# Kernel optimization log

Measured on AMD Instinct MI355X. Metric: run time of the kernel, lower is better.

Reference implementation:

```python
import jax, jax.numpy as jnp
import numpy as np

B, C, H, W = 4, 32, 64, 64
D_STATE, D_CONV = 16, 4


def _mamba(x, Win, convw, convb, Wx, Wdt, dtb, Alog, D, Wout, dt_rank):
    Bsz, L, _ = x.shape
    d_in, K = convw.shape
    xz = x @ Win.T                                  # (B, L, 2*d_inner)
    xc, z = xz[..., :d_in], xz[..., d_in:]
    xp = jnp.pad(xc, ((0, 0), (K - 1, 0), (0, 0)))  # causal left pad
    xconv = convb + sum(convw[:, k] * xp[:, k:k + L, :] for k in range(K))
    xa = jax.nn.silu(xconv)                         # (B, L, d_inner)
    xdbl = xa @ Wx.T                                # (B, L, dt_rank + 2*N)
    dt = jax.nn.softplus(xdbl[..., :dt_rank] @ Wdt.T + dtb)     # (B, L, d_inner)
    Bm = xdbl[..., dt_rank:dt_rank + D_STATE]                   # (B, L, N)
    Cm = xdbl[..., dt_rank + D_STATE:]                          # (B, L, N)
    A = -jnp.exp(Alog)                                          # (d_inner, N)
    dA = jnp.exp(dt[..., None] * A)                             # (B, L, d_inner, N)
    dBu = dt[..., None] * Bm[:, :, None, :] * xa[..., None]     # (B, L, d_inner, N)

    def step(h, inp):
        dA_t, dBu_t, C_t = inp
        h = dA_t * h + dBu_t
        return h, jnp.einsum('bdn,bn->bd', h, C_t)

    h0 = jnp.zeros((Bsz, d_in, D_STATE), x.dtype)
    _, ys = jax.lax.scan(step, h0, (dA.transpose(1, 0, 2, 3), dBu.transpose(1, 0, 2, 3), Cm.transpose(1, 0, 2)))
    y = ys.transpose(1, 0, 2) + D * xa
    return (y * jax.nn.silu(z)) @ Wout.T


def _line_seqs(x):
    # x: (B,C,H,W) -> four (B, H*W, C) directional scan orders
    hf = x.reshape(B, C, H * W).transpose(0, 2, 1)
    hb = hf[:, ::-1, :]
    wf = x.transpose(0, 1, 3, 2).reshape(B, C, H * W).transpose(0, 2, 1)
    wb = wf[:, ::-1, :]
    return hf, hb, wf, wb


def _oss(fo1, fo2, p1, p2):
    hf, hb, wf, wb = _line_seqs(fo1)
    fop = jnp.concatenate([hf, hb, wf, wb], axis=2)       # (B, HW, 4C)
    fop = _mamba(fop, *p1, dt_rank=8)
    fop = fop.reshape(B, H * W, 4, C).sum(2)              # (B, HW, C)
    fop = fop.transpose(0, 2, 1).reshape(B, C, H, W)
    residual = fop * fo2
    foc = residual.mean(axis=(2, 3)).reshape(B, C, 1)     # adaptive_avg_pool2d (1,1)
    foc = jnp.concatenate([foc, foc[:, ::-1, :]], axis=2) # (B, C, 2)
    foc = _mamba(foc, *p2, dt_rank=1)
    foc = foc.sum(2, keepdims=True)[..., None]            # (B, C, 1, 1)
    return foc * residual + residual


def setup_inputs() -> dict:
    key = jax.random.key(0)
    ks = jax.random.split(key, 18)
    def n(k, shape, s=0.02):
        return jax.random.normal(k, shape, jnp.float32) * s
    dm1, di1, dr1 = 4 * C, 8 * C, 8
    dm2, di2, dr2 = 2, 4, 1
    return {
        'fo1': jax.random.normal(ks[0], (B, C, H, W), jnp.float32),
        'fo2': jax.random.normal(ks[1], (B, C, H, W), jnp.float32),
        'm1_Win': n(ks[2], (2 * di1, dm1)),
        'm1_convw': n(ks[3], (di1, D_CONV), 0.2),
        'm1_convb': n(ks[4], (di1,), 0.1),
        'm1_Wx': n(ks[5], (dr1 + 2 * D_STATE, di1)),
        'm1_Wdt': n(ks[6], (di1, dr1), 0.1),
        'm1_dtb': n(ks[7], (di1,), 0.5),
        'm1_Alog': jnp.log(jnp.tile(jnp.arange(1, D_STATE + 1, dtype=jnp.float32), (di1, 1))),
        'm1_D': jnp.ones((di1,), jnp.float32),
        'm1_Wout': n(ks[8], (dm1, di1)),
        'm2_Win': n(ks[9], (2 * di2, dm2)),
        'm2_convw': n(ks[10], (di2, D_CONV), 0.2),
        'm2_convb': n(ks[11], (di2,), 0.1),
        'm2_Wx': n(ks[12], (dr2 + 2 * D_STATE, di2)),
        'm2_Wdt': n(ks[13], (di2, dr2), 0.1),
        'm2_dtb': n(ks[14], (di2,), 0.5),
        'm2_Alog': jnp.log(jnp.tile(jnp.arange(1, D_STATE + 1, dtype=jnp.float32), (di2, 1))),
        'm2_D': jnp.ones((di2,), jnp.float32),
        'm2_Wout': n(ks[15], (dm2, di2)),
    }


def reference(fo1, fo2, m1_Win, m1_convw, m1_convb, m1_Wx, m1_Wdt, m1_dtb, m1_Alog, m1_D, m1_Wout,
              m2_Win, m2_convw, m2_convb, m2_Wx, m2_Wdt, m2_dtb, m2_Alog, m2_D, m2_Wout):
    p1 = (m1_Win, m1_convw, m1_convb, m1_Wx, m1_Wdt, m1_dtb, m1_Alog, m1_D, m1_Wout)
    p2 = (m2_Win, m2_convw, m2_convb, m2_Wx, m2_Wdt, m2_dtb, m2_Alog, m2_D, m2_Wout)
    return _oss(fo1, fo2, p1, p2)
```

## Files before the change

kernel.cpp:

```cpp
#include <hip/hip_runtime.h>
#include <cstddef>


typedef __attribute__((ext_vector_type(8))) short short8v;
typedef __attribute__((ext_vector_type(4))) float f32x4;

__device__ __forceinline__ float siluf(float x) { return x / (1.f + __expf(-x)); }
__device__ __forceinline__ float softplusf(float x) { return (x > 20.f) ? x : log1pf(__expf(x)); }
__device__ __forceinline__ unsigned short f2bf(float f) {
  union { float f; unsigned int u; } v; v.f = f;
  unsigned int r = v.u + 0x7fff + ((v.u >> 16) & 1);
  return (unsigned short)(r >> 16);
}
__device__ __forceinline__ float bf2f(unsigned short u) {
  union { unsigned int i; float f; } v; v.i = ((unsigned int)u) << 16; return v.f;
}

__global__ __launch_bounds__(256) void k_build_fop(const float* __restrict__ fo1,
                                                   unsigned short* __restrict__ fopb) {
  int idx = blockIdx.x * 256 + threadIdx.x;
  int j = idx & 127;
  int l = (idx >> 7) & 4095;
  int b = idx >> 19;
  int g = j >> 5, c = j & 31;
  const float* base = fo1 + (size_t)(b * 32 + c) * 4096;
  int li;
  if (g == 0)      li = l;
  else if (g == 1) li = 4095 - l;
  else if (g == 2) li = ((l & 63) << 6) + (l >> 6);
  else { int i2 = 4095 - l; li = ((i2 & 63) << 6) + (i2 >> 6); }
  fopb[idx] = f2bf(base[li]);
}

__global__ __launch_bounds__(256) void k_gemm1_mfma(const unsigned short* __restrict__ A,
                                                    const float* __restrict__ Win,
                                                    unsigned short* __restrict__ xcb,
                                                    unsigned short* __restrict__ zb) {
  __shared__ unsigned short As[128][136];
  __shared__ unsigned short Bs[64][136];
  int t = threadIdx.x;
  int bm = blockIdx.x * 128, bn = blockIdx.y * 64;
#pragma unroll
  for (int it = 0; it < 8; ++it) {
    int idx = t + it * 256;
    int r = idx >> 4, kc = idx & 15;
    short8v v = *(const short8v*)&A[(size_t)(bm + r) * 128 + kc * 8];
    *(short8v*)&As[r][kc * 8] = v;
  }
#pragma unroll
  for (int it = 0; it < 8; ++it) {
    int idx = t + it * 256;
    int r = idx >> 5, kq = idx & 31;
    float4 w = *(const float4*)&Win[(size_t)(bn + r) * 128 + kq * 4];
    ushort4 h;
    h.x = f2bf(w.x); h.y = f2bf(w.y); h.z = f2bf(w.z); h.w = f2bf(w.w);
    *(ushort4*)&Bs[r][kq * 4] = h;
  }
  __syncthreads();
  int lane = t & 63, w = t >> 6;
  int wm = (w & 1) * 64, wn = (w >> 1) * 32;
  int lr = lane & 15, lg = lane >> 4;
  f32x4 acc[4][2] = {};
#pragma unroll
  for (int k0 = 0; k0 < 128; k0 += 32) {
    short8v a[4], b[2];
#pragma unroll
    for (int mf = 0; mf < 4; ++mf)
      a[mf] = *(const short8v*)&As[wm + mf * 16 + lr][k0 + lg * 8];
#pragma unroll
    for (int nf = 0; nf < 2; ++nf)
      b[nf] = *(const short8v*)&Bs[wn + nf * 16 + lr][k0 + lg * 8];
#pragma unroll
    for (int mf = 0; mf < 4; ++mf)
#pragma unroll
      for (int nf = 0; nf < 2; ++nf)
        acc[mf][nf] = __builtin_amdgcn_mfma_f32_16x16x32_bf16(a[mf], b[nf], acc[mf][nf], 0, 0, 0);
  }
  unsigned short* dst = (bn < 256) ? xcb : zb;
  int cb = (bn < 256) ? bn : (bn - 256);
#pragma unroll
  for (int mf = 0; mf < 4; ++mf)
#pragma unroll
    for (int nf = 0; nf < 2; ++nf)
#pragma unroll
      for (int r = 0; r < 4; ++r) {
        size_t row = bm + wm + mf * 16 + lg * 4 + r;
        dst[row * 256 + cb + wn + nf * 16 + lr] = f2bf(acc[mf][nf][r]);
      }
}

__global__ __launch_bounds__(256) void k_gemm2conv(const unsigned short* __restrict__ xcb,
                                                   const float* __restrict__ convw,
                                                   const float* __restrict__ convb,
                                                   const float* __restrict__ Wx,
                                                   unsigned short* __restrict__ xab,
                                                   float* __restrict__ xdbl) {
  __shared__ unsigned short xh[67][36];
  __shared__ float As[32][68];
  __shared__ float Ws[32][68];
  int t = threadIdx.x;
  int bm = blockIdx.x * 64;
  int b = bm >> 12, lloc0 = bm & 4095;
  int tx = t & 15, ty = t >> 4;
  int cc_conv = t & 31;
  float acc[4][4] = {};
  for (int k0 = 0; k0 < 256; k0 += 32) {
    for (int i = t; i < 1072; i += 256) {
      int rr = i >> 4, cc = i & 15;
      int lloc = lloc0 - 3 + rr;
      unsigned int val = 0;
      if (lloc >= 0)
        val = *(const unsigned int*)&xcb[((size_t)(b * 4096 + lloc)) * 256 + k0 + cc * 2];
      *(unsigned int*)&xh[rr][cc * 2] = val;
    }
#pragma unroll
    for (int it = 0; it < 2; ++it) {
      int idx = t + it * 256;
      int r = idx >> 3, kq = idx & 7;
      float4 w = make_float4(0.f, 0.f, 0.f, 0.f);
      if (r < 40) w = *(const float4*)&Wx[(size_t)r * 256 + k0 + kq * 4];
      Ws[kq * 4 + 0][r] = w.x; Ws[kq * 4 + 1][r] = w.y;
      Ws[kq * 4 + 2][r] = w.z; Ws[kq * 4 + 3][r] = w.w;
    }
    __syncthreads();
    {
      float4 w = *(const float4*)&convw[(k0 + cc_conv) * 4];
      float bias = convb[k0 + cc_conv];
#pragma unroll
      for (int it = 0; it < 8; ++it) {
        int r = (t >> 5) + it * 8;
        float a = bias;
        a = fmaf(w.x, bf2f(xh[r][cc_conv]), a);
        a = fmaf(w.y, bf2f(xh[r + 1][cc_conv]), a);
        a = fmaf(w.z, bf2f(xh[r + 2][cc_conv]), a);
        a = fmaf(w.w, bf2f(xh[r + 3][cc_conv]), a);
        float v = siluf(a);
        As[cc_conv][r] = v;
        xab[(size_t)(bm + r) * 256 + k0 + cc_conv] = f2bf(v);
      }
    }
    __syncthreads();
#pragma unroll
    for (int k = 0; k < 32; ++k) {
      float4 a = *(const float4*)&As[k][ty * 4];
      float4 w = *(const float4*)&Ws[k][tx * 4];
      float av[4] = {a.x, a.y, a.z, a.w};
      float wv[4] = {w.x, w.y, w.z, w.w};
#pragma unroll
      for (int i = 0; i < 4; ++i)
#pragma unroll
        for (int j = 0; j < 4; ++j)
          acc[i][j] = fmaf(av[i], wv[j], acc[i][j]);
    }
    __syncthreads();
  }
#pragma unroll
  for (int i = 0; i < 4; ++i) {
    size_t m = bm + ty * 4 + i;
#pragma unroll
    for (int j = 0; j < 4; ++j) {
      int n = tx * 4 + j;
      if (n < 40) xdbl[m * 40 + n] = acc[i][j];
    }
  }
}

__global__ __launch_bounds__(256) void k_scan_p1(const unsigned short* __restrict__ xab,
                                                 const float* __restrict__ xdbl,
                                                 const float* __restrict__ Wdt,
                                                 const float* __restrict__ dtb,
                                                 const float* __restrict__ Alog,
                                                 float* __restrict__ Pb,
                                                 float* __restrict__ Qb) {
  __shared__ f32x4 xrow[32][10];
  __shared__ float xas[32][256];
  int t = threadIdx.x;
  int blk = blockIdx.x;
  int ch = blk & 127, b = blk >> 7;
  size_t row0 = (size_t)b * 4096 + ch * 32;
  for (int i = t; i < 320; i += 256) {
    int s = i / 10, q = i - s * 10;
    xrow[s][q] = *(const f32x4*)&xdbl[(row0 + s) * 40 + q * 4];
  }
#pragma unroll
  for (int it = 0; it < 4; ++it) {
    int i = t + it * 256;
    int s = i >> 5, q = i & 31;
    short8v v = *(const short8v*)&xab[(row0 + s) * 256 + q * 8];
#pragma unroll
    for (int j = 0; j < 8; ++j) xas[s][q * 8 + j] = bf2f((unsigned short)v[j]);
  }
  __syncthreads();
  int d = t;
  f32x4 w0 = *(const f32x4*)&Wdt[d * 8];
  f32x4 w1 = *(const f32x4*)&Wdt[d * 8 + 4];
  float bias = dtb[d];
  float A[16], P[16], Q[16];
#pragma unroll
  for (int g = 0; g < 4; ++g) {
    f32x4 al = *(const f32x4*)&Alog[d * 16 + g * 4];
#pragma unroll
    for (int j = 0; j < 4; ++j) {
      A[g * 4 + j] = -__expf(al[j]);
      P[g * 4 + j] = 1.f;
      Q[g * 4 + j] = 0.f;
    }
  }
#pragma unroll 2
  for (int s = 0; s < 32; ++s) {
    f32x4 x0 = xrow[s][0], x1 = xrow[s][1];
    float v = bias;
#pragma unroll
    for (int j = 0; j < 4; ++j) v = fmaf(x0[j], w0[j], v);
#pragma unroll
    for (int j = 0; j < 4; ++j) v = fmaf(x1[j], w1[j], v);
    float ex = __expf(v);
    float dtv = (v > 20.f) ? v : __logf(1.f + ex);
    float du = dtv * xas[s][d];
    f32x4 bm[4];
#pragma unroll
    for (int g = 0; g < 4; ++g) bm[g] = xrow[s][2 + g];
#pragma unroll
    for (int n = 0; n < 16; ++n) {
      float e = __expf(dtv * A[n]);
      Q[n] = fmaf(e, Q[n], du * bm[n >> 2][n & 3]);
      P[n] *= e;
    }
  }
  size_t ob = (size_t)ch * 16384 + b * 4096 + d * 16;
#pragma unroll
  for (int g = 0; g < 4; ++g) {
    *(f32x4*)&Pb[ob + g * 4] = *(f32x4*)&P[g * 4];
    *(f32x4*)&Qb[ob + g * 4] = *(f32x4*)&Q[g * 4];
  }
}

__global__ __launch_bounds__(256) void k_scan_p2(const float* __restrict__ Pb,
                                                 const float* __restrict__ Qb,
                                                 float* __restrict__ Hin) {
  int t = blockIdx.x * 256 + threadIdx.x;
  float h = 0.f;
  size_t o = t;
#pragma unroll 8
  for (int ch = 0; ch < 128; ++ch) {
    Hin[o] = h;
    h = fmaf(Pb[o], h, Qb[o]);
    o += 16384;
  }
}

__global__ __launch_bounds__(256) void k_scan_p3(const unsigned short* __restrict__ xab,
                                                 const float* __restrict__ xdbl,
                                                 const float* __restrict__ Wdt,
                                                 const float* __restrict__ dtb,
                                                 const float* __restrict__ Alog,
                                                 const float* __restrict__ Hin,
                                                 const float* __restrict__ Dp,
                                                 const unsigned short* __restrict__ zb,
                                                 unsigned short* __restrict__ ym) {
  __shared__ f32x4 xrow[32][10];
  __shared__ float xas[32][256];
  int t = threadIdx.x;
  int blk = blockIdx.x;
  int ch = blk & 127, b = blk >> 7;
  size_t row0 = (size_t)b * 4096 + ch * 32;
  for (int i = t; i < 320; i += 256) {
    int s = i / 10, q = i - s * 10;
    xrow[s][q] = *(const f32x4*)&xdbl[(row0 + s) * 40 + q * 4];
  }
#pragma unroll
  for (int it = 0; it < 4; ++it) {
    int i = t + it * 256;
    int s = i >> 5, q = i & 31;
    short8v v = *(const short8v*)&xab[(row0 + s) * 256 + q * 8];
#pragma unroll
    for (int j = 0; j < 8; ++j) xas[s][q * 8 + j] = bf2f((unsigned short)v[j]);
  }
  __syncthreads();
  int d = t;
  f32x4 w0 = *(const f32x4*)&Wdt[d * 8];
  f32x4 w1 = *(const f32x4*)&Wdt[d * 8 + 4];
  float bias = dtb[d];
  float Dd = Dp[d];
  float A[16], h[16];
  size_t hb = (size_t)ch * 16384 + b * 4096 + d * 16;
#pragma unroll
  for (int g = 0; g < 4; ++g) {
    f32x4 al = *(const f32x4*)&Alog[d * 16 + g * 4];
    f32x4 hv = *(const f32x4*)&Hin[hb + g * 4];
#pragma unroll
    for (int j = 0; j < 4; ++j) {
      A[g * 4 + j] = -__expf(al[j]);
      h[g * 4 + j] = hv[j];
    }
  }
  const unsigned short* zp = zb + row0 * 256 + d;
  unsigned short* yo = ym + row0 * 256 + d;
#pragma unroll 2
  for (int s = 0; s < 32; ++s) {
    f32x4 x0 = xrow[s][0], x1 = xrow[s][1];
    float v = bias;
#pragma unroll
    for (int j = 0; j < 4; ++j) v = fmaf(x0[j], w0[j], v);
#pragma unroll
    for (int j = 0; j < 4; ++j) v = fmaf(x1[j], w1[j], v);
    float ex = __expf(v);
    float dtv = (v > 20.f) ? v : __logf(1.f + ex);
    float xav = xas[s][d];
    float du = dtv * xav;
    f32x4 bm[4], cm[4];
#pragma unroll
    for (int g = 0; g < 4; ++g) { bm[g] = xrow[s][2 + g]; cm[g] = xrow[s][6 + g]; }
    float y0 = 0.f, y1 = 0.f, y2 = 0.f, y3 = 0.f;
#pragma unroll
    for (int n = 0; n < 16; n += 4) {
      float e0 = __expf(dtv * A[n]);
      float e1 = __expf(dtv * A[n + 1]);
      float e2 = __expf(dtv * A[n + 2]);
      float e3 = __expf(dtv * A[n + 3]);
      f32x4 bv = bm[n >> 2], cv = cm[n >> 2];
      h[n]     = fmaf(e0, h[n],     du * bv[0]);
      h[n + 1] = fmaf(e1, h[n + 1], du * bv[1]);
      h[n + 2] = fmaf(e2, h[n + 2], du * bv[2]);
      h[n + 3] = fmaf(e3, h[n + 3], du * bv[3]);
      y0 = fmaf(h[n], cv[0], y0);
      y1 = fmaf(h[n + 1], cv[1], y1);
      y2 = fmaf(h[n + 2], cv[2], y2);
      y3 = fmaf(h[n + 3], cv[3], y3);
    }
    float y = (y0 + y1) + (y2 + y3) + Dd * xav;
    float z = bf2f(zp[s * 256]);
    yo[s * 256] = f2bf(y * siluf(z));
  }
}

__global__ __launch_bounds__(256) void k_gemm3res(const unsigned short* __restrict__ ym,
                                                  const float* __restrict__ Wout,
                                                  const float* __restrict__ fo2,
                                                  float* __restrict__ res,
                                                  float* __restrict__ focp) {
  __shared__ unsigned short As[64][264];
  __shared__ unsigned short Bs[32][264];
  __shared__ float fred[4][32];
  int t = threadIdx.x;
  int bm = blockIdx.x * 64;
#pragma unroll
  for (int it = 0; it < 8; ++it) {
    int idx = t + it * 256;
    int r = idx >> 5, kc = idx & 31;
    *(short8v*)&As[r][kc * 8] = *(const short8v*)&ym[(size_t)(bm + r) * 256 + kc * 8];
  }
#pragma unroll
  for (int it = 0; it < 32; ++it) {
    int idx = t + it * 256;
    int n = idx >> 8, k = idx & 255;
    float wv = Wout[(size_t)n * 256 + k] + Wout[(size_t)(n + 32) * 256 + k] +
               Wout[(size_t)(n + 64) * 256 + k] + Wout[(size_t)(n + 96) * 256 + k];
    Bs[n][k] = f2bf(wv);
  }
  __syncthreads();
  int lane = t & 63, w = t >> 6;
  int lr = lane & 15, lg = lane >> 4;
  f32x4 acc0 = {}, acc1 = {};
#pragma unroll
  for (int k0 = 0; k0 < 256; k0 += 32) {
    short8v a  = *(const short8v*)&As[w * 16 + lr][k0 + lg * 8];
    short8v b0 = *(const short8v*)&Bs[lr][k0 + lg * 8];
    short8v b1 = *(const short8v*)&Bs[16 + lr][k0 + lg * 8];
    acc0 = __builtin_amdgcn_mfma_f32_16x16x32_bf16(a, b0, acc0, 0, 0, 0);
    acc1 = __builtin_amdgcn_mfma_f32_16x16x32_bf16(a, b1, acc1, 0, 0, 0);
  }
  int b = bm >> 12;
  float ps0 = 0.f, ps1 = 0.f;
#pragma unroll
  for (int r = 0; r < 4; ++r) {
    int l = (bm + w * 16 + lg * 4 + r) & 4095;
    size_t ri0 = ((size_t)(b * 32 + lr)) * 4096 + l;
    size_t ri1 = ((size_t)(b * 32 + 16 + lr)) * 4096 + l;
    float v0 = acc0[r] * fo2[ri0];
    float v1 = acc1[r] * fo2[ri1];
    res[ri0] = v0; ps0 += v0;
    res[ri1] = v1; ps1 += v1;
  }
  ps0 += __shfl_xor(ps0, 16); ps0 += __shfl_xor(ps0, 32);
  ps1 += __shfl_xor(ps1, 16); ps1 += __shfl_xor(ps1, 32);
  if (lane < 16) { fred[w][lane] = ps0; fred[w][16 + lane] = ps1; }
  __syncthreads();
  if (t < 32)
    focp[((size_t)(b * 32 + t)) * 64 + (blockIdx.x & 63)] =
        fred[0][t] + fred[1][t] + fred[2][t] + fred[3][t];
}

__global__ __launch_bounds__(256) void k_mamba2(const float* __restrict__ focp,
                                                const float* __restrict__ Win2,
                                                const float* __restrict__ convw2,
                                                const float* __restrict__ convb2,
                                                const float* __restrict__ Wx2,
                                                const float* __restrict__ Wdt2,
                                                const float* __restrict__ dtb2,
                                                const float* __restrict__ Alog2,
                                                const float* __restrict__ D2,
                                                const float* __restrict__ Wout2,
                                                float* __restrict__ scale) {
  __shared__ float foc_s[128];
  __shared__ float xz2_s[4][32][8];
  __shared__ float xa2_s[4][32][4];
  __shared__ float xdbl2_s[4][32][33];
  __shared__ float dt2_s[4][32][4];
  __shared__ float ym2_s[4][32][4];
  int t = threadIdx.x;
  if (t < 128) {
    float s = 0.f;
    for (int k = 0; k < 64; ++k) s += focp[(size_t)t * 64 + k];
    foc_s[t] = s * (1.f / 4096.f);
  }
  __syncthreads();
  for (int i = t; i < 1024; i += 256) {
    int j = i & 7, l = (i >> 3) & 31, b = i >> 8;
    float x0 = foc_s[b * 32 + l], x1 = foc_s[b * 32 + 31 - l];
    xz2_s[b][l][j] = x0 * Win2[j * 2] + x1 * Win2[j * 2 + 1];
  }
  __syncthreads();
  for (int i = t; i < 512; i += 256) {
    int d = i & 3, l = (i >> 2) & 31, b = i >> 7;
    float acc = convb2[d];
#pragma unroll
    for (int k = 0; k < 4; ++k) {
      int ls = l + k - 3;
      if (ls >= 0) acc = fmaf(convw2[d * 4 + k], xz2_s[b][ls][d], acc);
    }
    xa2_s[b][l][d] = siluf(acc);
  }
  __syncthreads();
  for (int i = t; i < 4224; i += 256) {
    int r = i % 33, l = (i / 33) & 31, b = i / 1056;
    float s = 0.f;
#pragma unroll
    for (int d = 0; d < 4; ++d) s = fmaf(xa2_s[b][l][d], Wx2[r * 4 + d], s);
    xdbl2_s[b][l][r] = s;
  }
  __syncthreads();
  for (int i = t; i < 512; i += 256) {
    int d = i & 3, l = (i >> 2) & 31, b = i >> 7;
    float s = xdbl2_s[b][l][0] * Wdt2[d] + dtb2[d];
    dt2_s[b][l][d] = softplusf(s);
  }
  __syncthreads();
  {
    int n = t & 15, d = (t >> 4) & 3, b = t >> 6;
    float A = -__expf(Alog2[d * 16 + n]);
    float h = 0.f;
    for (int l = 0; l < 32; ++l) {
      float dtv = dt2_s[b][l][d];
      float xav = xa2_s[b][l][d];
      float e = __expf(dtv * A);
      h = fmaf(e, h, dtv * xdbl2_s[b][l][1 + n] * xav);
      float yp = h * xdbl2_s[b][l][17 + n];
      yp += __shfl_xor(yp, 1);
      yp += __shfl_xor(yp, 2);
      yp += __shfl_xor(yp, 4);
      yp += __shfl_xor(yp, 8);
      if (n == 0) {
        float z = xz2_s[b][l][4 + d];
        float y = yp + D2[d] * xav;
        ym2_s[b][l][d] = y * siluf(z);
      }
    }
  }
  __syncthreads();
  if (t < 128) {
    int l = t & 31, b = t >> 5;
    float s = 0.f;
#pragma unroll
    for (int d = 0; d < 4; ++d) s = fmaf(ym2_s[b][l][d], Wout2[d] + Wout2[4 + d], s);
    scale[t] = s;
  }
}

__global__ __launch_bounds__(256) void k_final(const float* __restrict__ res,
                                               const float* __restrict__ scale,
                                               float* __restrict__ out) {
  int idx = blockIdx.x * 256 + threadIdx.x;
  out[idx] = res[idx] * (1.f + scale[idx >> 12]);
}

extern "C" void kernel_launch(void* const* d_in, const int* in_sizes, int n_in,
                              void* d_out, int out_size, void* d_ws, size_t ws_size,
                              hipStream_t stream) {
  const float* fo1    = (const float*)d_in[0];
  const float* fo2    = (const float*)d_in[1];
  const float* Win    = (const float*)d_in[2];
  const float* convw  = (const float*)d_in[3];
  const float* convb  = (const float*)d_in[4];
  const float* Wx     = (const float*)d_in[5];
  const float* Wdt    = (const float*)d_in[6];
  const float* dtb    = (const float*)d_in[7];
  const float* Alog   = (const float*)d_in[8];
  const float* Dp     = (const float*)d_in[9];
  const float* Wout   = (const float*)d_in[10];
  const float* Win2   = (const float*)d_in[11];
  const float* convw2 = (const float*)d_in[12];
  const float* convb2 = (const float*)d_in[13];
  const float* Wx2    = (const float*)d_in[14];
  const float* Wdt2   = (const float*)d_in[15];
  const float* dtb2   = (const float*)d_in[16];
  const float* Alog2  = (const float*)d_in[17];
  const float* D2     = (const float*)d_in[18];
  const float* Wout2  = (const float*)d_in[19];

  float* ws = (float*)d_ws;
  unsigned short* fopb = (unsigned short*)ws;
  float* xdbl = ws;
  unsigned short* xcb = (unsigned short*)(ws + 1048576);
  unsigned short* zb  = (unsigned short*)(ws + 3145728);
  unsigned short* xab = (unsigned short*)(ws + 5242880);
  float* Pb   = ws + 7340032;
  float* Qb   = ws + 9437184;
  float* Hin  = ws + 11534336;
  unsigned short* ym = (unsigned short*)(ws + 13631488);
  float* res  = ws + 15728640;
  float* focp = ws + 16252928;
  float* scl  = ws + 16261120;
  if (ws_size < (size_t)16261248 * sizeof(float)) return;

  hipLaunchKernelGGL(k_build_fop, dim3(8192), dim3(256), 0, stream, fo1, fopb);
  hipLaunchKernelGGL(k_gemm1_mfma, dim3(128, 8), dim3(256), 0, stream, fopb, Win, xcb, zb);
  hipLaunchKernelGGL(k_gemm2conv, dim3(256), dim3(256), 0, stream,
                     xcb, convw, convb, Wx, xab, xdbl);
  hipLaunchKernelGGL(k_scan_p1, dim3(512), dim3(256), 0, stream,
                     xab, xdbl, Wdt, dtb, Alog, Pb, Qb);
  hipLaunchKernelGGL(k_scan_p2, dim3(64), dim3(256), 0, stream, Pb, Qb, Hin);
  hipLaunchKernelGGL(k_scan_p3, dim3(512), dim3(256), 0, stream,
                     xab, xdbl, Wdt, dtb, Alog, Hin, Dp, zb, ym);
  hipLaunchKernelGGL(k_gemm3res, dim3(256), dim3(256), 0, stream, ym, Wout, fo2, res, focp);
  hipLaunchKernelGGL(k_mamba2, dim3(1), dim3(256), 0, stream, focp, Win2, convw2, convb2,
                     Wx2, Wdt2, dtb2, Alog2, D2, Wout2, scl);
  hipLaunchKernelGGL(k_final, dim3(2048), dim3(256), 0, stream, res, scl, (float*)d_out);
}
```

Before: 134.8 us.

## Fuse three scan phases into one persistent kernel with grid barriers

Merges the chunk-local scan, the cross-chunk carry propagation, and the output scan into a single kernel of 512 blocks that sync through atomic-counter grid barriers. Each block keeps its staged xdbl/xa shared-memory tiles and the A coefficients across phases instead of reloading them in a third kernel. This removes two kernel launches and the repeated staging loads. The cost is a memset for the counters and reliance on all 512 blocks being co-resident (launch_bounds 256,2); if they are not, the spin-wait can deadlock until its iteration cap expires. The carry phase now uses only 32 threads per block.

```diff
diff --git a/kernel.cpp b/kernel.cpp
--- a/kernel.cpp
+++ b/kernel.cpp
@@ -14,6 +14,21 @@
 }
 __device__ __forceinline__ float bf2f(unsigned short u) {
   union { unsigned int i; float f; } v; v.i = ((unsigned int)u) << 16; return v.f;
+}
+
+__device__ __forceinline__ void grid_barrier(int* cnt, int target) {
+  __threadfence();
+  __syncthreads();
+  if (threadIdx.x == 0) {
+    __hip_atomic_fetch_add(cnt, 1, __ATOMIC_ACQ_REL, __HIP_MEMORY_SCOPE_AGENT);
+    int it = 0;
+    while (__hip_atomic_load(cnt, __ATOMIC_ACQUIRE, __HIP_MEMORY_SCOPE_AGENT) < target &&
+           it < (1 << 24)) {
+      __builtin_amdgcn_s_sleep(16);
+      ++it;
+    }
+  }
+  __syncthreads();
 }
 
 __global__ __launch_bounds__(256) void k_build_fop(const float* __restrict__ fo1,
@@ -165,13 +180,18 @@
   }
 }
 
-__global__ __launch_bounds__(256) void k_scan_p1(const unsigned short* __restrict__ xab,
-                                                 const float* __restrict__ xdbl,
-                                                 const float* __restrict__ Wdt,
-                                                 const float* __restrict__ dtb,
-                                                 const float* __restrict__ Alog,
-                                                 float* __restrict__ Pb,
-                                                 float* __restrict__ Qb) {
+__global__ __launch_bounds__(256, 2) void k_scan_fused(const unsigned short* __restrict__ xab,
+                                                       const float* __restrict__ xdbl,
+                                                       const float* __restrict__ Wdt,
+                                                       const float* __restrict__ dtb,
+                                                       const float* __restrict__ Alog,
+                                                       const float* __restrict__ Dp,
+                                                       const unsigned short* __restrict__ zb,
+                                                       float* __restrict__ Pb,
+                                                       float* __restrict__ Qb,
+                                                       float* __restrict__ Hin,
+                                                       int* __restrict__ cnt,
+                                                       unsigned short* __restrict__ ym) {
   __shared__ f32x4 xrow[32][10];
   __shared__ float xas[32][256];
   int t = threadIdx.x;
@@ -195,142 +215,108 @@
   f32x4 w0 = *(const f32x4*)&Wdt[d * 8];
   f32x4 w1 = *(const f32x4*)&Wdt[d * 8 + 4];
   float bias = dtb[d];
-  float A[16], P[16], Q[16];
-#pragma unroll
-  for (int g = 0; g < 4; ++g) {
-    f32x4 al = *(const f32x4*)&Alog[d * 16 + g * 4];
-#pragma unroll
-    for (int j = 0; j < 4; ++j) {
-      A[g * 4 + j] = -__expf(al[j]);
-      P[g * 4 + j] = 1.f;
-      Q[g * 4 + j] = 0.f;
-    }
-  }
+  float A[16];
+  {
+    float P[16], Q[16];
+#pragma unroll
+    for (int g = 0; g < 4; ++g) {
+      f32x4 al = *(const f32x4*)&Alog[d * 16 + g * 4];
+#pragma unroll
+      for (int j = 0; j < 4; ++j) {
+        A[g * 4 + j] = -__expf(al[j]);
+        P[g * 4 + j] = 1.f;
+        Q[g * 4 + j] = 0.f;
+      }
+    }
 #pragma unroll 2
-  for (int s = 0; s < 32; ++s) {
-    f32x4 x0 = xrow[s][0], x1 = xrow[s][1];
-    float v = bias;
-#pragma unroll
-    for (int j = 0; j < 4; ++j) v = fmaf(x0[j], w0[j], v);
-#pragma unroll
-    for (int j = 0; j < 4; ++j) v = fmaf(x1[j], w1[j], v);
-    float ex = __expf(v);
-    float dtv = (v > 20.f) ? v : __logf(1.f + ex);
-    float du = dtv * xas[s][d];
-    f32x4 bm[4];
-#pragma unroll
-    for (int g = 0; g < 4; ++g) bm[g] = xrow[s][2 + g];
-#pragma unroll
-    for (int n = 0; n < 16; ++n) {
-      float e = __expf(dtv * A[n]);
-      Q[n] = fmaf(e, Q[n], du * bm[n >> 2][n & 3]);
-      P[n] *= e;
-    }
-  }
-  size_t ob = (size_t)ch * 16384 + b * 4096 + d * 16;
-#pragma unroll
-  for (int g = 0; g < 4; ++g) {
-    *(f32x4*)&Pb[ob + g * 4] = *(f32x4*)&P[g * 4];
-    *(f32x4*)&Qb[ob + g * 4] = *(f32x4*)&Q[g * 4];
-  }
-}
-
-__global__ __launch_bounds__(256) void k_scan_p2(const float* __restrict__ Pb,
-                                                 const float* __restrict__ Qb,
-                                                 float* __restrict__ Hin) {
-  int t = blockIdx.x * 256 + threadIdx.x;
-  float h = 0.f;
-  size_t o = t;
+    for (int s = 0; s < 32; ++s) {
+      f32x4 x0 = xrow[s][0], x1 = xrow[s][1];
+      float v = bias;
+#pragma unroll
+      for (int j = 0; j < 4; ++j) v = fmaf(x0[j], w0[j], v);
+#pragma unroll
+      for (int j = 0; j < 4; ++j) v = fmaf(x1[j], w1[j], v);
+      float ex = __expf(v);
+      float dtv = (v > 20.f) ? v : __logf(1.f + ex);
+      float du = dtv * xas[s][d];
+      f32x4 bm[4];
+#pragma unroll
+      for (int g = 0; g < 4; ++g) bm[g] = xrow[s][2 + g];
+#pragma unroll
+      for (int n = 0; n < 16; ++n) {
+        float e = __expf(dtv * A[n]);
+        Q[n] = fmaf(e, Q[n], du * bm[n >> 2][n & 3]);
+        P[n] *= e;
+      }
+    }
+    size_t ob = (size_t)ch * 16384 + b * 4096 + d * 16;
+#pragma unroll
+    for (int g = 0; g < 4; ++g) {
+      *(f32x4*)&Pb[ob + g * 4] = *(f32x4*)&P[g * 4];
+      *(f32x4*)&Qb[ob + g * 4] = *(f32x4*)&Q[g * 4];
+    }
+  }
+  grid_barrier(cnt, 512);
+  if (t < 32) {
+    int col = blk * 32 + t;
+    float h = 0.f;
+    size_t o = col;
 #pragma unroll 8
-  for (int ch = 0; ch < 128; ++ch) {
-    Hin[o] = h;
-    h = fmaf(Pb[o], h, Qb[o]);
-    o += 16384;
-  }
-}
-
-__global__ __launch_bounds__(256) void k_scan_p3(const unsigned short* __restrict__ xab,
-                                                 const float* __restrict__ xdbl,
-                                                 const float* __restrict__ Wdt,
-                                                 const float* __restrict__ dtb,
-                                                 const float* __restrict__ Alog,
-                                                 const float* __restrict__ Hin,
-                                                 const float* __restrict__ Dp,
-                                                 const unsigned short* __restrict__ zb,
-                                                 unsigned short* __restrict__ ym) {
-  __shared__ f32x4 xrow[32][10];
-  __shared__ float xas[32][256];
-  int t = threadIdx.x;
-  int blk = blockIdx.x;
-  int ch = blk & 127, b = blk >> 7;
-  size_t row0 = (size_t)b * 4096 + ch * 32;
-  for (int i = t; i < 320; i += 256) {
-    int s = i / 10, q = i - s * 10;
-    xrow[s][q] = *(const f32x4*)&xdbl[(row0 + s) * 40 + q * 4];
-  }
-#pragma unroll
-  for (int it = 0; it < 4; ++it) {
-    int i = t + it * 256;
-    int s = i >> 5, q = i & 31;
-    short8v v = *(const short8v*)&xab[(row0 + s) * 256 + q * 8];
-#pragma unroll
-    for (int j = 0; j < 8; ++j) xas[s][q * 8 + j] = bf2f((unsigned short)v[j]);
-  }
-  __syncthreads();
-  int d = t;
-  f32x4 w0 = *(const f32x4*)&Wdt[d * 8];
-  f32x4 w1 = *(const f32x4*)&Wdt[d * 8 + 4];
-  float bias = dtb[d];
-  float Dd = Dp[d];
-  float A[16], h[16];
-  size_t hb = (size_t)ch * 16384 + b * 4096 + d * 16;
-#pragma unroll
-  for (int g = 0; g < 4; ++g) {
-    f32x4 al = *(const f32x4*)&Alog[d * 16 + g * 4];
-    f32x4 hv = *(const f32x4*)&Hin[hb + g * 4];
-#pragma unroll
-    for (int j = 0; j < 4; ++j) {
-      A[g * 4 + j] = -__expf(al[j]);
-      h[g * 4 + j] = hv[j];
-    }
-  }
-  const unsigned short* zp = zb + row0 * 256 + d;
-  unsigned short* yo = ym + row0 * 256 + d;
+    for (int c2 = 0; c2 < 128; ++c2) {
+      Hin[o] = h;
+      h = fmaf(Pb[o], h, Qb[o]);
+      o += 16384;
+    }
+  }
+  grid_barrier(cnt + 1, 512);
+  {
+    float Dd = Dp[d];
+    float h[16];
+    size_t hb = (size_t)ch * 16384 + b * 4096 + d * 16;
+#pragma unroll
+    for (int g = 0; g < 4; ++g) {
+      f32x4 hv = *(const f32x4*)&Hin[hb + g * 4];
+#pragma unroll
+      for (int j = 0; j < 4; ++j) h[g * 4 + j] = hv[j];
+    }
+    const unsigned short* zp = zb + row0 * 256 + d;
+    unsigned short* yo = ym + row0 * 256 + d;
 #pragma unroll 2
-  for (int s = 0; s < 32; ++s) {
-    f32x4 x0 = xrow[s][0], x1 = xrow[s][1];
-    float v = bias;
-#pragma unroll
-    for (int j = 0; j < 4; ++j) v = fmaf(x0[j], w0[j], v);
-#pragma unroll
-    for (int j = 0; j < 4; ++j) v = fmaf(x1[j], w1[j], v);
-    float ex = __expf(v);
-    float dtv = (v > 20.f) ? v : __logf(1.f + ex);
-    float xav = xas[s][d];
-    float du = dtv * xav;
-    f32x4 bm[4], cm[4];
-#pragma unroll
-    for (int g = 0; g < 4; ++g) { bm[g] = xrow[s][2 + g]; cm[g] = xrow[s][6 + g]; }
-    float y0 = 0.f, y1 = 0.f, y2 = 0.f, y3 = 0.f;
-#pragma unroll
-    for (int n = 0; n < 16; n += 4) {
-      float e0 = __expf(dtv * A[n]);
-      float e1 = __expf(dtv * A[n + 1]);
-      float e2 = __expf(dtv * A[n + 2]);
-      float e3 = __expf(dtv * A[n + 3]);
-      f32x4 bv = bm[n >> 2], cv = cm[n >> 2];
-      h[n]     = fmaf(e0, h[n],     du * bv[0]);
-      h[n + 1] = fmaf(e1, h[n + 1], du * bv[1]);
-      h[n + 2] = fmaf(e2, h[n + 2], du * bv[2]);
-      h[n + 3] = fmaf(e3, h[n + 3], du * bv[3]);
-      y0 = fmaf(h[n], cv[0], y0);
-      y1 = fmaf(h[n + 1], cv[1], y1);
-      y2 = fmaf(h[n + 2], cv[2], y2);
-      y3 = fmaf(h[n + 3], cv[3], y3);
-    }
-    float y = (y0 + y1) + (y2 + y3) + Dd * xav;
-    float z = bf2f(zp[s * 256]);
-    yo[s * 256] = f2bf(y * siluf(z));
+    for (int s = 0; s < 32; ++s) {
+      f32x4 x0 = xrow[s][0], x1 = xrow[s][1];
+      float v = bias;
+#pragma unroll
+      for (int j = 0; j < 4; ++j) v = fmaf(x0[j], w0[j], v);
+#pragma unroll
+      for (int j = 0; j < 4; ++j) v = fmaf(x1[j], w1[j], v);
+      float ex = __expf(v);
+      float dtv = (v > 20.f) ? v : __logf(1.f + ex);
+      float xav = xas[s][d];
+      float du = dtv * xav;
+      f32x4 bm[4], cm[4];
+#pragma unroll
+      for (int g = 0; g < 4; ++g) { bm[g] = xrow[s][2 + g]; cm[g] = xrow[s][6 + g]; }
+      float y0 = 0.f, y1 = 0.f, y2 = 0.f, y3 = 0.f;
+#pragma unroll
+      for (int n = 0; n < 16; n += 4) {
+        float e0 = __expf(dtv * A[n]);
+        float e1 = __expf(dtv * A[n + 1]);
+        float e2 = __expf(dtv * A[n + 2]);
+        float e3 = __expf(dtv * A[n + 3]);
+        f32x4 bv = bm[n >> 2], cv = cm[n >> 2];
+        h[n]     = fmaf(e0, h[n],     du * bv[0]);
+        h[n + 1] = fmaf(e1, h[n + 1], du * bv[1]);
+        h[n + 2] = fmaf(e2, h[n + 2], du * bv[2]);
+        h[n + 3] = fmaf(e3, h[n + 3], du * bv[3]);
+        y0 = fmaf(h[n], cv[0], y0);
+        y1 = fmaf(h[n + 1], cv[1], y1);
+        y2 = fmaf(h[n + 2], cv[2], y2);
+        y3 = fmaf(h[n + 3], cv[3], y3);
+      }
+      float y = (y0 + y1) + (y2 + y3) + Dd * xav;
+      float z = bf2f(zp[s * 256]);
+      yo[s * 256] = f2bf(y * siluf(z));
+    }
   }
 }
 
@@ -521,17 +507,16 @@
   float* res  = ws + 15728640;
   float* focp = ws + 16252928;
   float* scl  = ws + 16261120;
-  if (ws_size < (size_t)16261248 * sizeof(float)) return;
-
+  int*   cnt  = (int*)(ws + 16261248);
+  if (ws_size < (size_t)16261504 * sizeof(float)) return;
+
+  hipMemsetAsync(cnt, 0, 2 * sizeof(int), stream);
   hipLaunchKernelGGL(k_build_fop, dim3(8192), dim3(256), 0, stream, fo1, fopb);
   hipLaunchKernelGGL(k_gemm1_mfma, dim3(128, 8), dim3(256), 0, stream, fopb, Win, xcb, zb);
   hipLaunchKernelGGL(k_gemm2conv, dim3(256), dim3(256), 0, stream,
                      xcb, convw, convb, Wx, xab, xdbl);
-  hipLaunchKernelGGL(k_scan_p1, dim3(512), dim3(256), 0, stream,
-                     xab, xdbl, Wdt, dtb, Alog, Pb, Qb);
-  hipLaunchKernelGGL(k_scan_p2, dim3(64), dim3(256), 0, stream, Pb, Qb, Hin);
-  hipLaunchKernelGGL(k_scan_p3, dim3(512), dim3(256), 0, stream,
-                     xab, xdbl, Wdt, dtb, Alog, Hin, Dp, zb, ym);
+  hipLaunchKernelGGL(k_scan_fused, dim3(512), dim3(256), 0, stream,
+                     xab, xdbl, Wdt, dtb, Alog, Dp, zb, Pb, Qb, Hin, cnt, ym);
   hipLaunchKernelGGL(k_gemm3res, dim3(256), dim3(256), 0, stream, ym, Wout, fo2, res, focp);
   hipLaunchKernelGGL(k_mamba2, dim3(1), dim3(256), 0, stream, focp, Win2, convw2, convb2,
                      Wx2, Wdt2, dtb2, Alog2, D2, Wout2, scl);
```

Result: slower. 315.2 us (+133.8%).
